# Performance work log

Measured on AMD Instinct MI355X. Metric: run time of the kernel, lower is better.

Reference implementation:

```python
import jax, jax.numpy as jnp
import numpy as np
import math

IN_FEATURES = 4096
OUT_FEATURES = 4096
RANK = 16
B, S = 4, 2048


def setup_inputs() -> dict:
    key = jax.random.key(0)
    k_x, k_w, k_b, k_a = jax.random.split(key, 4)
    x = jax.random.normal(k_x, (B, S, IN_FEATURES), dtype=jnp.float32)
    # base linear params (torch nn.Linear default init scale)
    bound_w = 1.0 / math.sqrt(IN_FEATURES)
    W = jax.random.uniform(k_w, (OUT_FEATURES, IN_FEATURES), minval=-bound_w, maxval=bound_w, dtype=jnp.float32)
    bias = jax.random.uniform(k_b, (OUT_FEATURES,), minval=-bound_w, maxval=bound_w, dtype=jnp.float32)
    # lora_A: kaiming_uniform_(a=sqrt(5)) over shape (out, rank) -> fan_in = rank
    bound_a = 1.0 / math.sqrt(RANK)
    lora_A = jax.random.uniform(k_a, (OUT_FEATURES, RANK), minval=-bound_a, maxval=bound_a, dtype=jnp.float32)
    # lora_B initialized to zeros in the module; use small random values so the
    # delta path is numerically exercised in the baseline.
    lora_B = jax.random.normal(jax.random.fold_in(key, 7), (RANK, IN_FEATURES), dtype=jnp.float32) * 0.01
    return {"x": x, "W": W, "bias": bias, "lora_A": lora_A, "lora_B": lora_B}


def reference(x, W, bias, lora_A, lora_B):
    # Faithful to the torch module: materialize the full [out, in] LoRA delta
    # (lora_A @ lora_B), then apply base linear + delta linear.
    lora_update = lora_A @ lora_B                      # [out, in]
    base = jnp.einsum('bsi,oi->bso', x, W) + bias      # base_layer(x)
    delta = jnp.einsum('bsi,oi->bso', x, lora_update)  # F.linear(x, lora_update)
    return base + delta
```

## Files before the change

kernel.cpp:

```cpp
#include <hip/hip_runtime.h>
#include <hip/hip_bf16.h>
#include <stdint.h>


typedef unsigned short u16;
typedef __attribute__((ext_vector_type(8))) u16 u16x8;
typedef __attribute__((ext_vector_type(4))) u16 u16x4;
typedef __attribute__((ext_vector_type(8))) __bf16 bf16x8;
typedef __attribute__((ext_vector_type(4))) float f32x4;

#define IN_F 4096
#define OUT_F 4096
#define MTOT 8192
#define RANK 16
#define NT64 192

__device__ __forceinline__ u16 f2bf(float f) {
  unsigned u = __float_as_uint(f);
  unsigned r = u + 0x7FFFu + ((u >> 16) & 1u);
  return (u16)(r >> 16);
}
__device__ __forceinline__ float bf2f(u16 h) {
  return __uint_as_float(((unsigned)h) << 16);
}

__global__ __launch_bounds__(256) void prep_kernel(
    const float* __restrict__ x, const float* __restrict__ W,
    const float* __restrict__ lA, const float* __restrict__ lB,
    u16* __restrict__ xhi, u16* __restrict__ xlo, u16* __restrict__ whi,
    u16* __restrict__ wlo) {
  const int t = threadIdx.x;
  if (blockIdx.x < 3072) {
    const int n4 = (MTOT * IN_F) / 4;
    int idx = blockIdx.x * 256 + t;
    for (; idx < n4; idx += 3072 * 256) {
      float4 v = ((const float4*)x)[idx];
      u16x4 h, l;
      h.x = f2bf(v.x); l.x = f2bf(v.x - bf2f(h.x));
      h.y = f2bf(v.y); l.y = f2bf(v.y - bf2f(h.y));
      h.z = f2bf(v.z); l.z = f2bf(v.z - bf2f(h.z));
      h.w = f2bf(v.w); l.w = f2bf(v.w - bf2f(h.w));
      ((u16x4*)xhi)[idx] = h;
      ((u16x4*)xlo)[idx] = l;
    }
  } else {
    const int bw = blockIdx.x - 3072;
    const int strip = bw & 31;
    const int og = bw >> 5;
    const int i4 = strip * 32 + (t & 31);
    float4 lbr[RANK];
#pragma unroll
    for (int r = 0; r < RANK; ++r)
      lbr[r] = ((const float4*)lB)[r * (IN_F / 4) + i4];
#pragma unroll 1
    for (int j = 0; j < 16; ++j) {
      const int o = og * 128 + (t >> 5) + 8 * j;
      float a[RANK];
#pragma unroll
      for (int q = 0; q < 4; ++q) {
        float4 av = ((const float4*)lA)[o * (RANK / 4) + q];
        a[q * 4 + 0] = av.x; a[q * 4 + 1] = av.y;
        a[q * 4 + 2] = av.z; a[q * 4 + 3] = av.w;
      }
      float4 acc = ((const float4*)W)[o * (IN_F / 4) + i4];
#pragma unroll
      for (int r = 0; r < RANK; ++r) {
        acc.x += a[r] * lbr[r].x; acc.y += a[r] * lbr[r].y;
        acc.z += a[r] * lbr[r].z; acc.w += a[r] * lbr[r].w;
      }
      u16x4 h, l;
      h.x = f2bf(acc.x); l.x = f2bf(acc.x - bf2f(h.x));
      h.y = f2bf(acc.y); l.y = f2bf(acc.y - bf2f(h.y));
      h.z = f2bf(acc.z); l.z = f2bf(acc.z - bf2f(h.z));
      h.w = f2bf(acc.w); l.w = f2bf(acc.w - bf2f(h.w));
      ((u16x4*)whi)[o * (IN_F / 4) + i4] = h;
      ((u16x4*)wlo)[o * (IN_F / 4) + i4] = l;
    }
  }
}

#define GLD_LDS16(g, l)                                                  \
  __builtin_amdgcn_global_load_lds(                                      \
      (const __attribute__((address_space(1))) void*)(g),                \
      (__attribute__((address_space(3))) void*)(l), 16, 0, 0)

__global__ __launch_bounds__(512, 2) void gemm_pipe_kernel(
    const u16* __restrict__ Xhi, const u16* __restrict__ Xlo,
    const u16* __restrict__ Whi, const u16* __restrict__ Wlo,
    const float* __restrict__ bias, float* __restrict__ out) {
  __shared__ __align__(16) u16 LDS[65536];

  const int t = threadIdx.x;
  const int lane = t & 63;
  const int wv = t >> 6;
  const int wm = wv >> 2;
  const int wn = wv & 3;
  const int fr = lane & 15;
  const int fq = lane >> 4;

  const int wg = ((blockIdx.x & 7) << 6) | (blockIdx.x >> 3);
  const int m0 = (wg >> 4) * 256;
  const int n0 = (wg & 15) * 256;

  const int scol = ((t & 7) ^ ((t >> 3) & 7)) * 8;
  const size_t aoff = (size_t)(m0 + (t >> 3)) * IN_F + scol;
  const size_t boff = (size_t)(n0 + (t >> 3)) * IN_F + scol;

  const int lk0 = fr * 64 + (((0 * 4 + fq) ^ (fr & 7)) * 8);
  const int lk1 = fr * 64 + (((1 * 4 + fq) ^ (fr & 7)) * 8);

  f32x4 acc[8][4];
#pragma unroll
  for (int i = 0; i < 8; ++i)
#pragma unroll
    for (int j = 0; j < 4; ++j) {
      acc[i][j][0] = 0.f; acc[i][j][1] = 0.f;
      acc[i][j][2] = 0.f; acc[i][j][3] = 0.f;
    }

  auto stageA = [&](int g, int sbuf) {
    const int sg = g >> 6;
    const u16* ap = (sg == 1) ? Xlo : Xhi;
    const int k0 = (g & 63) << 6;
    u16* dA = (u16*)&LDS[sbuf * 32768];
    const u16* s = ap + aoff + k0;
    GLD_LDS16(s, dA + t * 8);
    GLD_LDS16(s + (size_t)64 * IN_F, dA + (512 + t) * 8);
    GLD_LDS16(s + (size_t)128 * IN_F, dA + (1024 + t) * 8);
    GLD_LDS16(s + (size_t)192 * IN_F, dA + (1536 + t) * 8);
  };
  auto stageB = [&](int g, int sbuf) {
    const int sg = g >> 6;
    const u16* bp = (sg == 2) ? Wlo : Whi;
    const int k0 = (g & 63) << 6;
    u16* dB = (u16*)&LDS[sbuf * 32768 + 16384];
    const u16* s = bp + boff + k0;
    GLD_LDS16(s, dB + t * 8);
    GLD_LDS16(s + (size_t)64 * IN_F, dB + (512 + t) * 8);
    GLD_LDS16(s + (size_t)128 * IN_F, dB + (1024 + t) * 8);
    GLD_LDS16(s + (size_t)192 * IN_F, dB + (1536 + t) * 8);
  };

#define MFMA_Q(AARR, AIDX, BARR, BIDX, ACC)                             \
  ACC = __builtin_amdgcn_mfma_f32_16x16x32_bf16(                        \
      __builtin_bit_cast(bf16x8, AARR[AIDX]),                           \
      __builtin_bit_cast(bf16x8, BARR[BIDX]), ACC, 0, 0, 0)

  stageA(0, 0); stageB(0, 0);

#pragma unroll 1
  for (int tt = 0; tt < NT64; ++tt) {
    const int buf = tt & 1;
    const u16* Ab = &LDS[buf * 32768];
    const u16* Bb = Ab + 16384;
    int g = tt + 1;
    if (g >= NT64) g = NT64 - 1;
    const int sbuf = buf ^ 1;

    asm volatile("s_waitcnt vmcnt(0)" ::: "memory");
    __builtin_amdgcn_s_barrier();
    __builtin_amdgcn_sched_barrier(0);

    u16x8 af[8], af2[8], bf0[4], bf1[4];

#pragma unroll
    for (int mi = 0; mi < 4; ++mi) {
      af[mi * 2 + 0] = *(const u16x8*)&Ab[wm * 8192 + mi * 1024 + lk0];
      af[mi * 2 + 1] = *(const u16x8*)&Ab[wm * 8192 + mi * 1024 + lk1];
    }
#pragma unroll
    for (int ci = 0; ci < 2; ++ci) {
      bf0[ci * 2 + 0] = *(const u16x8*)&Bb[wn * 4096 + ci * 1024 + lk0];
      bf0[ci * 2 + 1] = *(const u16x8*)&Bb[wn * 4096 + ci * 1024 + lk1];
      bf1[ci * 2 + 0] = *(const u16x8*)&Bb[wn * 4096 + 2048 + ci * 1024 + lk0];
      bf1[ci * 2 + 1] = *(const u16x8*)&Bb[wn * 4096 + 2048 + ci * 1024 + lk1];
    }
    stageA(g, sbuf);
    __builtin_amdgcn_sched_barrier(0);

    __builtin_amdgcn_s_setprio(1);
#pragma unroll
    for (int mi = 0; mi < 4; ++mi)
#pragma unroll
      for (int ci = 0; ci < 2; ++ci) {
        MFMA_Q(af, mi * 2 + 0, bf0, ci * 2 + 0, acc[mi][ci]);
        MFMA_Q(af, mi * 2 + 1, bf0, ci * 2 + 1, acc[mi][ci]);
      }
    __builtin_amdgcn_s_setprio(0);
    __builtin_amdgcn_sched_barrier(0);

#pragma unroll
    for (int mi = 0; mi < 4; ++mi) {
      af2[mi * 2 + 0] = *(const u16x8*)&Ab[wm * 8192 + 4096 + mi * 1024 + lk0];
      af2[mi * 2 + 1] = *(const u16x8*)&Ab[wm * 8192 + 4096 + mi * 1024 + lk1];
    }
    stageB(g, sbuf);
    __builtin_amdgcn_sched_barrier(0);

    __builtin_amdgcn_s_setprio(1);
#pragma unroll
    for (int mi = 0; mi < 4; ++mi)
#pragma unroll
      for (int ci = 0; ci < 2; ++ci) {
        MFMA_Q(af, mi * 2 + 0, bf1, ci * 2 + 0, acc[mi][2 + ci]);
        MFMA_Q(af, mi * 2 + 1, bf1, ci * 2 + 1, acc[mi][2 + ci]);
      }
    __builtin_amdgcn_s_setprio(0);
    __builtin_amdgcn_sched_barrier(0);

    __builtin_amdgcn_s_setprio(1);
#pragma unroll
    for (int mi = 0; mi < 4; ++mi)
#pragma unroll
      for (int ci = 0; ci < 2; ++ci) {
        MFMA_Q(af2, mi * 2 + 0, bf1, ci * 2 + 0, acc[4 + mi][2 + ci]);
        MFMA_Q(af2, mi * 2 + 1, bf1, ci * 2 + 1, acc[4 + mi][2 + ci]);
      }
#pragma unroll
    for (int mi = 0; mi < 4; ++mi)
#pragma unroll
      for (int ci = 0; ci < 2; ++ci) {
        MFMA_Q(af2, mi * 2 + 0, bf0, ci * 2 + 0, acc[4 + mi][ci]);
        MFMA_Q(af2, mi * 2 + 1, bf0, ci * 2 + 1, acc[4 + mi][ci]);
      }
    __builtin_amdgcn_s_setprio(0);
  }

#pragma unroll
  for (int a = 0; a < 8; ++a) {
    const int row = m0 + wm * 128 + (a >> 2) * 64 + (a & 3) * 16 + fq * 4;
#pragma unroll
    for (int b = 0; b < 4; ++b) {
      const int col = n0 + wn * 64 + (b >> 1) * 32 + (b & 1) * 16 + fr;
      const float bb = bias[col];
#pragma unroll
      for (int r = 0; r < 4; ++r)
        out[(size_t)(row + r) * OUT_F + col] = acc[a][b][r] + bb;
    }
  }
#undef MFMA_Q
}

__global__ __launch_bounds__(256) void gemm_f32_fallback(
    const float* __restrict__ X, const float* __restrict__ W,
    const float* __restrict__ lA, const float* __restrict__ lB,
    const float* __restrict__ bias, float* __restrict__ out) {
  __shared__ __align__(16) float Xs[64 * 32];
  __shared__ __align__(16) float Ws[64 * 32];
  const int t = threadIdx.x;
  const int bm = blockIdx.x & 127;
  const int bn = blockIdx.x >> 7;
  const int m0 = bm * 64, n0 = bn * 64;
  const int tx = t & 15, ty = t >> 4;
  float acc[4][4] = {};
  for (int k0 = 0; k0 < IN_F; k0 += 32) {
    __syncthreads();
#pragma unroll
    for (int q = 0; q < 2; ++q) {
      const int e4 = t * 2 + q;
      const int row = e4 >> 3;
      const int col = (e4 & 7) * 4;
      float4 xv = *(const float4*)(X + (size_t)(m0 + row) * IN_F + k0 + col);
      *(float4*)(Xs + row * 32 + col) = xv;
      float4 wv = *(const float4*)(W + (size_t)(n0 + row) * IN_F + k0 + col);
#pragma unroll
      for (int r = 0; r < RANK; ++r) {
        const float a = lA[(n0 + row) * RANK + r];
        const float4 b = *(const float4*)(lB + (size_t)r * IN_F + k0 + col);
        wv.x += a * b.x; wv.y += a * b.y; wv.z += a * b.z; wv.w += a * b.w;
      }
      *(float4*)(Ws + row * 32 + col) = wv;
    }
    __syncthreads();
#pragma unroll
    for (int kk = 0; kk < 32; ++kk) {
      float xr[4], wcol[4];
#pragma unroll
      for (int i = 0; i < 4; ++i) xr[i] = Xs[(ty * 4 + i) * 32 + kk];
#pragma unroll
      for (int j = 0; j < 4; ++j) wcol[j] = Ws[(tx * 4 + j) * 32 + kk];
#pragma unroll
      for (int i = 0; i < 4; ++i)
#pragma unroll
        for (int j = 0; j < 4; ++j) acc[i][j] += xr[i] * wcol[j];
    }
  }
#pragma unroll
  for (int i = 0; i < 4; ++i) {
    const int row = m0 + ty * 4 + i;
#pragma unroll
    for (int j = 0; j < 4; ++j) {
      const int col = n0 + tx * 4 + j;
      out[(size_t)row * OUT_F + col] = acc[i][j] + bias[col];
    }
  }
}

extern "C" void kernel_launch(void* const* d_in, const int* in_sizes, int n_in,
                              void* d_out, int out_size, void* d_ws,
                              size_t ws_size, hipStream_t stream) {
  const float* x    = (const float*)d_in[0];
  const float* W    = (const float*)d_in[1];
  const float* bias = (const float*)d_in[2];
  const float* lA   = (const float*)d_in[3];
  const float* lB   = (const float*)d_in[4];
  float* out = (float*)d_out;

  const size_t MK = (size_t)MTOT * IN_F;
  const size_t NK = (size_t)OUT_F * IN_F;
  const size_t need = (MK * 2 + NK * 2) * sizeof(u16);

  if (ws_size >= need) {
    u16* Xhi = (u16*)d_ws;
    u16* Xlo = Xhi + MK;
    u16* Whi = Xlo + MK;
    u16* Wlo = Whi + NK;
    prep_kernel<<<4096, 256, 0, stream>>>(x, W, lA, lB, Xhi, Xlo, Whi, Wlo);
    gemm_pipe_kernel<<<512, 512, 0, stream>>>(Xhi, Xlo, Whi, Wlo, bias, out);
  } else {
    gemm_f32_fallback<<<128 * 64, 256, 0, stream>>>(x, W, lA, lB, bias, out);
  }
}
```

Baseline: 883.3 us.

## Load W operand directly from global into registers, halving LDS usage

Each wave now loads its B (weight) fragments straight from global memory into registers, one tile ahead, using double-buffered register arrays. The LDS staging of B is removed, which halves shared memory per block and drops the B LDS reads. The main loop is unrolled by two to alternate the register buffers. In exchange, each wave fetches its own B rows with no sharing across the waves that use the same columns, so global/L2 traffic and register pressure go up and occupancy may suffer.

```diff
diff --git a/kernel.cpp b/kernel.cpp
--- a/kernel.cpp
+++ b/kernel.cpp
@@ -88,7 +88,7 @@
     const u16* __restrict__ Xhi, const u16* __restrict__ Xlo,
     const u16* __restrict__ Whi, const u16* __restrict__ Wlo,
     const float* __restrict__ bias, float* __restrict__ out) {
-  __shared__ __align__(16) u16 LDS[65536];
+  __shared__ __align__(16) u16 LDS[32768];
 
   const int t = threadIdx.x;
   const int lane = t & 63;
@@ -104,10 +104,11 @@
 
   const int scol = ((t & 7) ^ ((t >> 3) & 7)) * 8;
   const size_t aoff = (size_t)(m0 + (t >> 3)) * IN_F + scol;
-  const size_t boff = (size_t)(n0 + (t >> 3)) * IN_F + scol;
 
   const int lk0 = fr * 64 + (((0 * 4 + fq) ^ (fr & 7)) * 8);
   const int lk1 = fr * 64 + (((1 * 4 + fq) ^ (fr & 7)) * 8);
+
+  const size_t bOff = (size_t)(n0 + wn * 64 + fr) * IN_F + fq * 8;
 
   f32x4 acc[8][4];
 #pragma unroll
@@ -122,37 +123,37 @@
     const int sg = g >> 6;
     const u16* ap = (sg == 1) ? Xlo : Xhi;
     const int k0 = (g & 63) << 6;
-    u16* dA = (u16*)&LDS[sbuf * 32768];
+    u16* dA = (u16*)&LDS[sbuf * 16384];
     const u16* s = ap + aoff + k0;
     GLD_LDS16(s, dA + t * 8);
     GLD_LDS16(s + (size_t)64 * IN_F, dA + (512 + t) * 8);
     GLD_LDS16(s + (size_t)128 * IN_F, dA + (1024 + t) * 8);
     GLD_LDS16(s + (size_t)192 * IN_F, dA + (1536 + t) * 8);
   };
-  auto stageB = [&](int g, int sbuf) {
-    const int sg = g >> 6;
-    const u16* bp = (sg == 2) ? Wlo : Whi;
-    const int k0 = (g & 63) << 6;
-    u16* dB = (u16*)&LDS[sbuf * 32768 + 16384];
-    const u16* s = bp + boff + k0;
-    GLD_LDS16(s, dB + t * 8);
-    GLD_LDS16(s + (size_t)64 * IN_F, dB + (512 + t) * 8);
-    GLD_LDS16(s + (size_t)128 * IN_F, dB + (1024 + t) * 8);
-    GLD_LDS16(s + (size_t)192 * IN_F, dB + (1536 + t) * 8);
+  auto loadB = [&](int g, u16x8 (&dst)[8]) {
+    const u16* bp = ((g >> 6) == 2) ? Wlo : Whi;
+    const u16* s = bp + bOff + ((g & 63) << 6);
+#pragma unroll
+    for (int ni = 0; ni < 4; ++ni)
+#pragma unroll
+      for (int ks = 0; ks < 2; ++ks)
+        dst[ni * 2 + ks] =
+            *(const u16x8*)(s + (size_t)ni * 16 * IN_F + ks * 32);
   };
 
-#define MFMA_Q(AARR, AIDX, BARR, BIDX, ACC)                             \
+#define MFMA_Q(AIDX, BARR, BIDX, ACC)                                   \
   ACC = __builtin_amdgcn_mfma_f32_16x16x32_bf16(                        \
-      __builtin_bit_cast(bf16x8, AARR[AIDX]),                           \
+      __builtin_bit_cast(bf16x8, af[AIDX]),                             \
       __builtin_bit_cast(bf16x8, BARR[BIDX]), ACC, 0, 0, 0)
 
-  stageA(0, 0); stageB(0, 0);
-
-#pragma unroll 1
-  for (int tt = 0; tt < NT64; ++tt) {
+  u16x8 Bx[8], By[8];
+
+  stageA(0, 0);
+  loadB(0, Bx);
+
+  auto tile = [&](int tt, u16x8 (&Bc)[8], u16x8 (&Bn)[8]) {
     const int buf = tt & 1;
-    const u16* Ab = &LDS[buf * 32768];
-    const u16* Bb = Ab + 16384;
+    const u16* Ab = &LDS[buf * 16384];
     int g = tt + 1;
     if (g >= NT64) g = NT64 - 1;
     const int sbuf = buf ^ 1;
@@ -161,20 +162,14 @@
     __builtin_amdgcn_s_barrier();
     __builtin_amdgcn_sched_barrier(0);
 
-    u16x8 af[8], af2[8], bf0[4], bf1[4];
+    u16x8 af[8];
 
 #pragma unroll
     for (int mi = 0; mi < 4; ++mi) {
       af[mi * 2 + 0] = *(const u16x8*)&Ab[wm * 8192 + mi * 1024 + lk0];
       af[mi * 2 + 1] = *(const u16x8*)&Ab[wm * 8192 + mi * 1024 + lk1];
     }
-#pragma unroll
-    for (int ci = 0; ci < 2; ++ci) {
-      bf0[ci * 2 + 0] = *(const u16x8*)&Bb[wn * 4096 + ci * 1024 + lk0];
-      bf0[ci * 2 + 1] = *(const u16x8*)&Bb[wn * 4096 + ci * 1024 + lk1];
-      bf1[ci * 2 + 0] = *(const u16x8*)&Bb[wn * 4096 + 2048 + ci * 1024 + lk0];
-      bf1[ci * 2 + 1] = *(const u16x8*)&Bb[wn * 4096 + 2048 + ci * 1024 + lk1];
-    }
+    loadB(g, Bn);
     stageA(g, sbuf);
     __builtin_amdgcn_sched_barrier(0);
 
@@ -183,18 +178,28 @@
     for (int mi = 0; mi < 4; ++mi)
 #pragma unroll
       for (int ci = 0; ci < 2; ++ci) {
-        MFMA_Q(af, mi * 2 + 0, bf0, ci * 2 + 0, acc[mi][ci]);
-        MFMA_Q(af, mi * 2 + 1, bf0, ci * 2 + 1, acc[mi][ci]);
+        MFMA_Q(mi * 2 + 0, Bc, ci * 2 + 0, acc[mi][ci]);
+        MFMA_Q(mi * 2 + 1, Bc, ci * 2 + 1, acc[mi][ci]);
       }
     __builtin_amdgcn_s_setprio(0);
     __builtin_amdgcn_sched_barrier(0);
 
+    __builtin_amdgcn_s_setprio(1);
+#pragma unroll
+    for (int mi = 0; mi < 4; ++mi)
+#pragma unroll
+      for (int ci = 0; ci < 2; ++ci) {
+        MFMA_Q(mi * 2 + 0, Bc, 4 + ci * 2 + 0, acc[mi][2 + ci]);
+        MFMA_Q(mi * 2 + 1, Bc, 4 + ci * 2 + 1, acc[mi][2 + ci]);
+      }
+    __builtin_amdgcn_s_setprio(0);
+    __builtin_amdgcn_sched_barrier(0);
+
 #pragma unroll
     for (int mi = 0; mi < 4; ++mi) {
-      af2[mi * 2 + 0] = *(const u16x8*)&Ab[wm * 8192 + 4096 + mi * 1024 + lk0];
-      af2[mi * 2 + 1] = *(const u16x8*)&Ab[wm * 8192 + 4096 + mi * 1024 + lk1];
-    }
-    stageB(g, sbuf);
+      af[mi * 2 + 0] = *(const u16x8*)&Ab[wm * 8192 + 4096 + mi * 1024 + lk0];
+      af[mi * 2 + 1] = *(const u16x8*)&Ab[wm * 8192 + 4096 + mi * 1024 + lk1];
+    }
     __builtin_amdgcn_sched_barrier(0);
 
     __builtin_amdgcn_s_setprio(1);
@@ -202,28 +207,23 @@
     for (int mi = 0; mi < 4; ++mi)
 #pragma unroll
       for (int ci = 0; ci < 2; ++ci) {
-        MFMA_Q(af, mi * 2 + 0, bf1, ci * 2 + 0, acc[mi][2 + ci]);
-        MFMA_Q(af, mi * 2 + 1, bf1, ci * 2 + 1, acc[mi][2 + ci]);
+        MFMA_Q(mi * 2 + 0, Bc, 4 + ci * 2 + 0, acc[4 + mi][2 + ci]);
+        MFMA_Q(mi * 2 + 1, Bc, 4 + ci * 2 + 1, acc[4 + mi][2 + ci]);
+      }
+#pragma unroll
+    for (int mi = 0; mi < 4; ++mi)
+#pragma unroll
+      for (int ci = 0; ci < 2; ++ci) {
+        MFMA_Q(mi * 2 + 0, Bc, ci * 2 + 0, acc[4 + mi][ci]);
+        MFMA_Q(mi * 2 + 1, Bc, ci * 2 + 1, acc[4 + mi][ci]);
       }
     __builtin_amdgcn_s_setprio(0);
-    __builtin_amdgcn_sched_barrier(0);
-
-    __builtin_amdgcn_s_setprio(1);
-#pragma unroll
-    for (int mi = 0; mi < 4; ++mi)
-#pragma unroll
-      for (int ci = 0; ci < 2; ++ci) {
-        MFMA_Q(af2, mi * 2 + 0, bf1, ci * 2 + 0, acc[4 + mi][2 + ci]);
-        MFMA_Q(af2, mi * 2 + 1, bf1, ci * 2 + 1, acc[4 + mi][2 + ci]);
-      }
-#pragma unroll
-    for (int mi = 0; mi < 4; ++mi)
-#pragma unroll
-      for (int ci = 0; ci < 2; ++ci) {
-        MFMA_Q(af2, mi * 2 + 0, bf0, ci * 2 + 0, acc[4 + mi][ci]);
-        MFMA_Q(af2, mi * 2 + 1, bf0, ci * 2 + 1, acc[4 + mi][ci]);
-      }
-    __builtin_amdgcn_s_setprio(0);
+  };
+
+#pragma unroll 1
+  for (int p = 0; p < NT64 / 2; ++p) {
+    tile(2 * p + 0, Bx, By);
+    tile(2 * p + 1, By, Bx);
   }
 
 #pragma unroll
```

Result: slower. 1.315 ms (+48.9%).

## Switch GEMM to 32x32x16 MFMA tiles and widen x conversion grid

Applied to the files above, without the earlier changes.

The main GEMM now uses 32x32x16 bf16 MFMA instead of 16x16x32. Each wave holds a 4x2 set of 16-float accumulators and reads LDS fragments with a new swizzled k-index layout. The larger MFMA shape halves the instruction count and raises operand reuse per fragment load, while keeping the same register footprint. The prep kernel also gets more blocks for the x hi/lo split, which adds parallelism to that memory-bound pass.

```diff
diff --git a/kernel.cpp b/kernel.cpp
--- a/kernel.cpp
+++ b/kernel.cpp
@@ -7,7 +7,7 @@
 typedef __attribute__((ext_vector_type(8))) u16 u16x8;
 typedef __attribute__((ext_vector_type(4))) u16 u16x4;
 typedef __attribute__((ext_vector_type(8))) __bf16 bf16x8;
-typedef __attribute__((ext_vector_type(4))) float f32x4;
+typedef __attribute__((ext_vector_type(16))) float f32x16;
 
 #define IN_F 4096
 #define OUT_F 4096
@@ -30,10 +30,10 @@
     u16* __restrict__ xhi, u16* __restrict__ xlo, u16* __restrict__ whi,
     u16* __restrict__ wlo) {
   const int t = threadIdx.x;
-  if (blockIdx.x < 3072) {
+  if (blockIdx.x < 7168) {
     const int n4 = (MTOT * IN_F) / 4;
     int idx = blockIdx.x * 256 + t;
-    for (; idx < n4; idx += 3072 * 256) {
+    for (; idx < n4; idx += 7168 * 256) {
       float4 v = ((const float4*)x)[idx];
       u16x4 h, l;
       h.x = f2bf(v.x); l.x = f2bf(v.x - bf2f(h.x));
@@ -44,7 +44,7 @@
       ((u16x4*)xlo)[idx] = l;
     }
   } else {
-    const int bw = blockIdx.x - 3072;
+    const int bw = blockIdx.x - 7168;
     const int strip = bw & 31;
     const int og = bw >> 5;
     const int i4 = strip * 32 + (t & 31);
@@ -95,8 +95,8 @@
   const int wv = t >> 6;
   const int wm = wv >> 2;
   const int wn = wv & 3;
-  const int fr = lane & 15;
-  const int fq = lane >> 4;
+  const int rl = lane & 31;
+  const int kb = lane >> 5;
 
   const int wg = ((blockIdx.x & 7) << 6) | (blockIdx.x >> 3);
   const int m0 = (wg >> 4) * 256;
@@ -106,17 +106,18 @@
   const size_t aoff = (size_t)(m0 + (t >> 3)) * IN_F + scol;
   const size_t boff = (size_t)(n0 + (t >> 3)) * IN_F + scol;
 
-  const int lk0 = fr * 64 + (((0 * 4 + fq) ^ (fr & 7)) * 8);
-  const int lk1 = fr * 64 + (((1 * 4 + fq) ^ (fr & 7)) * 8);
-
-  f32x4 acc[8][4];
-#pragma unroll
-  for (int i = 0; i < 8; ++i)
-#pragma unroll
-    for (int j = 0; j < 4; ++j) {
-      acc[i][j][0] = 0.f; acc[i][j][1] = 0.f;
-      acc[i][j][2] = 0.f; acc[i][j][3] = 0.f;
-    }
+  int lkk[4];
+#pragma unroll
+  for (int ks = 0; ks < 4; ++ks)
+    lkk[ks] = rl * 64 + (((ks * 2 + kb) ^ (rl & 7)) * 8);
+
+  f32x16 acc[4][2];
+#pragma unroll
+  for (int i = 0; i < 4; ++i)
+#pragma unroll
+    for (int j = 0; j < 2; ++j)
+#pragma unroll
+      for (int k = 0; k < 16; ++k) acc[i][j][k] = 0.f;
 
   auto stageA = [&](int g, int sbuf) {
     const int sg = g >> 6;
@@ -141,8 +142,8 @@
     GLD_LDS16(s + (size_t)192 * IN_F, dB + (1536 + t) * 8);
   };
 
-#define MFMA_Q(AARR, AIDX, BARR, BIDX, ACC)                             \
-  ACC = __builtin_amdgcn_mfma_f32_16x16x32_bf16(                        \
+#define MFMA32(AARR, AIDX, BARR, BIDX, ACC)                             \
+  ACC = __builtin_amdgcn_mfma_f32_32x32x16_bf16(                        \
       __builtin_bit_cast(bf16x8, AARR[AIDX]),                           \
       __builtin_bit_cast(bf16x8, BARR[BIDX]), ACC, 0, 0, 0)
 
@@ -164,81 +165,74 @@
     u16x8 af[8], af2[8], bf0[4], bf1[4];
 
 #pragma unroll
-    for (int mi = 0; mi < 4; ++mi) {
-      af[mi * 2 + 0] = *(const u16x8*)&Ab[wm * 8192 + mi * 1024 + lk0];
-      af[mi * 2 + 1] = *(const u16x8*)&Ab[wm * 8192 + mi * 1024 + lk1];
-    }
+    for (int mi = 0; mi < 2; ++mi)
+#pragma unroll
+      for (int ks = 0; ks < 4; ++ks)
+        af[mi * 4 + ks] =
+            *(const u16x8*)&Ab[wm * 8192 + mi * 2048 + lkk[ks]];
+#pragma unroll
+    for (int ks = 0; ks < 4; ++ks) {
+      bf0[ks] = *(const u16x8*)&Bb[wn * 4096 + lkk[ks]];
+      bf1[ks] = *(const u16x8*)&Bb[wn * 4096 + 2048 + lkk[ks]];
+    }
+    stageA(g, sbuf);
+    __builtin_amdgcn_sched_barrier(0);
+
+    __builtin_amdgcn_s_setprio(1);
+#pragma unroll
+    for (int ks = 0; ks < 4; ++ks)
+#pragma unroll
+      for (int mi = 0; mi < 2; ++mi)
+        MFMA32(af, mi * 4 + ks, bf0, ks, acc[mi][0]);
+    __builtin_amdgcn_s_setprio(0);
+    __builtin_amdgcn_sched_barrier(0);
+
+#pragma unroll
+    for (int mi = 0; mi < 2; ++mi)
+#pragma unroll
+      for (int ks = 0; ks < 4; ++ks)
+        af2[mi * 4 + ks] =
+            *(const u16x8*)&Ab[wm * 8192 + (2 + mi) * 2048 + lkk[ks]];
+    stageB(g, sbuf);
+    __builtin_amdgcn_sched_barrier(0);
+
+    __builtin_amdgcn_s_setprio(1);
+#pragma unroll
+    for (int ks = 0; ks < 4; ++ks)
+#pragma unroll
+      for (int mi = 0; mi < 2; ++mi)
+        MFMA32(af, mi * 4 + ks, bf1, ks, acc[mi][1]);
+    __builtin_amdgcn_s_setprio(0);
+    __builtin_amdgcn_sched_barrier(0);
+
+    __builtin_amdgcn_s_setprio(1);
+#pragma unroll
+    for (int ks = 0; ks < 4; ++ks)
+#pragma unroll
+      for (int mi = 0; mi < 2; ++mi)
+        MFMA32(af2, mi * 4 + ks, bf1, ks, acc[2 + mi][1]);
+#pragma unroll
+    for (int ks = 0; ks < 4; ++ks)
+#pragma unroll
+      for (int mi = 0; mi < 2; ++mi)
+        MFMA32(af2, mi * 4 + ks, bf0, ks, acc[2 + mi][0]);
+    __builtin_amdgcn_s_setprio(0);
+  }
+
+#pragma unroll
+  for (int mi = 0; mi < 4; ++mi)
 #pragma unroll
     for (int ci = 0; ci < 2; ++ci) {
-      bf0[ci * 2 + 0] = *(const u16x8*)&Bb[wn * 4096 + ci * 1024 + lk0];
-      bf0[ci * 2 + 1] = *(const u16x8*)&Bb[wn * 4096 + ci * 1024 + lk1];
-      bf1[ci * 2 + 0] = *(const u16x8*)&Bb[wn * 4096 + 2048 + ci * 1024 + lk0];
-      bf1[ci * 2 + 1] = *(const u16x8*)&Bb[wn * 4096 + 2048 + ci * 1024 + lk1];
-    }
-    stageA(g, sbuf);
-    __builtin_amdgcn_sched_barrier(0);
-
-    __builtin_amdgcn_s_setprio(1);
-#pragma unroll
-    for (int mi = 0; mi < 4; ++mi)
-#pragma unroll
-      for (int ci = 0; ci < 2; ++ci) {
-        MFMA_Q(af, mi * 2 + 0, bf0, ci * 2 + 0, acc[mi][ci]);
-        MFMA_Q(af, mi * 2 + 1, bf0, ci * 2 + 1, acc[mi][ci]);
+      const int col = n0 + wn * 64 + ci * 32 + rl;
+      const float bb = bias[col];
+#pragma unroll
+      for (int reg = 0; reg < 16; ++reg) {
+        const int row =
+            m0 + wm * 128 + mi * 32 + (reg & 3) + 8 * (reg >> 2) + 4 * kb;
+        out[(size_t)row * OUT_F + col] = acc[mi][ci][reg] + bb;
       }
-    __builtin_amdgcn_s_setprio(0);
-    __builtin_amdgcn_sched_barrier(0);
-
-#pragma unroll
-    for (int mi = 0; mi < 4; ++mi) {
-      af2[mi * 2 + 0] = *(const u16x8*)&Ab[wm * 8192 + 4096 + mi * 1024 + lk0];
-      af2[mi * 2 + 1] = *(const u16x8*)&Ab[wm * 8192 + 4096 + mi * 1024 + lk1];
-    }
-    stageB(g, sbuf);
-    __builtin_amdgcn_sched_barrier(0);
-
-    __builtin_amdgcn_s_setprio(1);
-#pragma unroll
-    for (int mi = 0; mi < 4; ++mi)
-#pragma unroll
-      for (int ci = 0; ci < 2; ++ci) {
-        MFMA_Q(af, mi * 2 + 0, bf1, ci * 2 + 0, acc[mi][2 + ci]);
-        MFMA_Q(af, mi * 2 + 1, bf1, ci * 2 + 1, acc[mi][2 + ci]);
-      }
-    __builtin_amdgcn_s_setprio(0);
-    __builtin_amdgcn_sched_barrier(0);
-
-    __builtin_amdgcn_s_setprio(1);
-#pragma unroll
-    for (int mi = 0; mi < 4; ++mi)
-#pragma unroll
-      for (int ci = 0; ci < 2; ++ci) {
-        MFMA_Q(af2, mi * 2 + 0, bf1, ci * 2 + 0, acc[4 + mi][2 + ci]);
-        MFMA_Q(af2, mi * 2 + 1, bf1, ci * 2 + 1, acc[4 + mi][2 + ci]);
-      }
-#pragma unroll
-    for (int mi = 0; mi < 4; ++mi)
-#pragma unroll
-      for (int ci = 0; ci < 2; ++ci) {
-        MFMA_Q(af2, mi * 2 + 0, bf0, ci * 2 + 0, acc[4 + mi][ci]);
-        MFMA_Q(af2, mi * 2 + 1, bf0, ci * 2 + 1, acc[4 + mi][ci]);
-      }
-    __builtin_amdgcn_s_setprio(0);
-  }
-
-#pragma unroll
-  for (int a = 0; a < 8; ++a) {
-    const int row = m0 + wm * 128 + (a >> 2) * 64 + (a & 3) * 16 + fq * 4;
-#pragma unroll
-    for (int b = 0; b < 4; ++b) {
-      const int col = n0 + wn * 64 + (b >> 1) * 32 + (b & 1) * 16 + fr;
-      const float bb = bias[col];
-#pragma unroll
-      for (int r = 0; r < 4; ++r)
-        out[(size_t)(row + r) * OUT_F + col] = acc[a][b][r] + bb;
-    }
-  }
-#undef MFMA_Q
+    }
+#undef MFMA32
 }
 
 __global__ __launch_bounds__(256) void gemm_f32_fallback(
@@ -315,7 +309,7 @@
     u16* Xlo = Xhi + MK;
     u16* Whi = Xlo + MK;
     u16* Wlo = Whi + NK;
-    prep_kernel<<<4096, 256, 0, stream>>>(x, W, lA, lB, Xhi, Xlo, Whi, Wlo);
+    prep_kernel<<<8192, 256, 0, stream>>>(x, W, lA, lB, Xhi, Xlo, Whi, Wlo);
     gemm_pipe_kernel<<<512, 512, 0, stream>>>(Xhi, Xlo, Whi, Wlo, bias, out);
   } else {
     gemm_f32_fallback<<<128 * 64, 256, 0, stream>>>(x, W, lA, lB, bias, out);
```

Measured after the change: 1.079 ms. +22.2%, slower.
